# Optimization experiments

Hardware: AMD Instinct MI355X
Metric: run time of the kernel (lower is better)

Reference implementation:

```python
import jax, jax.numpy as jnp
import numpy as np

H = 16  # num_heads
D = 1024  # hidden_dim
HD = D // H  # head_dim


def setup_inputs() -> dict:
    key = jax.random.key(0)
    ks = jax.random.split(key, 12)
    B, S = 2, 2048
    x = jax.random.normal(ks[0], (B, S, D), dtype=jnp.float32)
    attention_bias = jax.random.normal(ks[1], (H, S, S), dtype=jnp.float32) * 0.1
    # padding mask: True = masked; last (S - len) positions padded, no all-masked rows
    lengths = jax.random.randint(ks[2], (B,), S // 2, S + 1)
    key_padding_mask = jnp.arange(S)[None, :] >= lengths[:, None]  # [B, S] bool
    s = 1.0 / np.sqrt(D)
    Wq = jax.random.normal(ks[3], (D, D), dtype=jnp.float32) * s
    bq = jnp.zeros((D,), dtype=jnp.float32)
    Wk = jax.random.normal(ks[4], (D, D), dtype=jnp.float32) * s
    bk = jnp.zeros((D,), dtype=jnp.float32)
    Wv = jax.random.normal(ks[5], (D, D), dtype=jnp.float32) * s
    bv = jnp.zeros((D,), dtype=jnp.float32)
    Wo = jax.random.normal(ks[6], (D, D), dtype=jnp.float32) * s
    bo = jnp.zeros((D,), dtype=jnp.float32)
    return {"x": x, "attention_bias": attention_bias, "key_padding_mask": key_padding_mask,
            "Wq": Wq, "bq": bq, "Wk": Wk, "bk": bk, "Wv": Wv, "bv": bv, "Wo": Wo, "bo": bo}


def reference(x, attention_bias, key_padding_mask, Wq, bq, Wk, bk, Wv, bv, Wo, bo):
    B, S, _ = x.shape
    scale = HD ** (-0.5)

    def shape_heads(t):  # [B,S,D] -> [B,H,S,HD]
        return t.reshape(B, S, H, HD).transpose(0, 2, 1, 3)

    q = shape_heads(x @ Wq + bq)
    k = shape_heads(x @ Wk + bk)
    v = shape_heads(x @ Wv + bv)

    attn = jnp.einsum('bhqd,bhkd->bhqk', q, k) * scale  # [B,H,S,S]
    attn = attn + attention_bias[None]
    attn = jnp.where(key_padding_mask[:, None, None, :], -jnp.inf, attn)

    # handle fully-masked rows: zero their logits pre-softmax, zero weights after
    all_masked = jnp.all(key_padding_mask, axis=1)  # [B]
    bad = all_masked[:, None, None, None]
    safe_attn = jnp.where(bad, 0.0, attn)
    weights = jax.nn.softmax(safe_attn, axis=-1)
    weights = jnp.where(bad, 0.0, weights)

    context = jnp.einsum('bhqk,bhkd->bhqd', weights, v)  # [B,H,S,HD]
    context = context.transpose(0, 2, 1, 3).reshape(B, S, D)
    return context @ Wo + bo
```

## Files before the change

kernel.cpp:

```cpp
#include <hip/hip_runtime.h>
#include <hip/hip_bf16.h>
#include <stdint.h>

#define BB 2
#define SS 2048
#define DDIM 1024
#define HH 16
#define HDIM 64

typedef __hip_bfloat16 bf16;
typedef __bf16 bf16x8 __attribute__((ext_vector_type(8)));
typedef float f32x4 __attribute__((ext_vector_type(4)));
typedef short short8 __attribute__((ext_vector_type(8)));
typedef short s16x4 __attribute__((ext_vector_type(4)));

static __device__ __forceinline__ f32x4 mfma16(bf16x8 a, bf16x8 b, f32x4 c) {
  return __builtin_amdgcn_mfma_f32_16x16x32_bf16(a, b, c, 0, 0, 0);
}

static __device__ __forceinline__ void gload_lds16(const void* g, void* l) {
  __builtin_amdgcn_global_load_lds(
      (const __attribute__((address_space(1))) void*)g,
      (__attribute__((address_space(3))) void*)l, 16, 0, 0);
}

__global__ __launch_bounds__(256) void cvt_k(const float* __restrict__ src,
                                             bf16* __restrict__ dst) {
  const int base = (blockIdx.x * 256 + threadIdx.x) * 8;
  float4 a = *reinterpret_cast<const float4*>(src + base);
  float4 b = *reinterpret_cast<const float4*>(src + base + 4);
  union {
    bf16 h[8];
    short8 v;
  } u;
  u.h[0] = __float2bfloat16(a.x);
  u.h[1] = __float2bfloat16(a.y);
  u.h[2] = __float2bfloat16(a.z);
  u.h[3] = __float2bfloat16(a.w);
  u.h[4] = __float2bfloat16(b.x);
  u.h[5] = __float2bfloat16(b.y);
  u.h[6] = __float2bfloat16(b.z);
  u.h[7] = __float2bfloat16(b.w);
  *reinterpret_cast<short8*>(dst + base) = u.v;
}

__global__ __launch_bounds__(256) void transpose_cvt_k(
    const float* __restrict__ src, bf16* __restrict__ dst) {
  __shared__ float tile[64][65];
  const int t = threadIdx.x;
  const int r = t >> 2, c0 = (t & 3) * 16;
  const int bx = blockIdx.x * 64, by = blockIdx.y * 64;
  const float* sp = src + (size_t)(by + r) * DDIM + bx + c0;
#pragma unroll
  for (int j = 0; j < 16; ++j) tile[r][c0 + j] = sp[j];
  __syncthreads();
  bf16* dp = dst + (size_t)(bx + r) * DDIM + by + c0;
#pragma unroll
  for (int j = 0; j < 16; ++j) dp[j] = __float2bfloat16(tile[c0 + j][r]);
}

__global__ __launch_bounds__(64) void mask_pack_k(
    const int* __restrict__ kpm, unsigned long long* __restrict__ mb) {
  const int i = threadIdx.x;
  const int b = i >> 5, c = i & 31;
  unsigned long long bits = 0ull;
  for (int j = 0; j < 64; ++j)
    bits |= (unsigned long long)(kpm[b * SS + c * 64 + j] != 0) << j;
  mb[i] = bits;
}

template <int MODE>
__global__ __launch_bounds__(256, 2) void gemm_bt(
    const bf16* __restrict__ A, const bf16* __restrict__ Bt,
    const float* __restrict__ b0, const float* __restrict__ b1,
    const float* __restrict__ b2, bf16* __restrict__ O0,
    bf16* __restrict__ O1, bf16* __restrict__ O2, float* __restrict__ Of) {
  constexpr int Kd = DDIM;
  __shared__ bf16x8 lA[128 * 8];
  __shared__ bf16x8 lB[128 * 8];
  const int tid = threadIdx.x;
  const int wave = tid >> 6, lane = tid & 63;
  const int l15 = lane & 15, l4 = lane >> 4;
  const int wm = wave >> 1, wn = wave & 1;
  const int m0 = blockIdx.x * 128, n0 = blockIdx.y * 128;
  const f32x4 z = {0.f, 0.f, 0.f, 0.f};
  f32x4 acc[4][4];
#pragma unroll
  for (int i = 0; i < 4; ++i)
#pragma unroll
    for (int j = 0; j < 4; ++j) acc[i][j] = z;

  for (int k0 = 0; k0 < Kd; k0 += 64) {
#pragma unroll
    for (int j = 0; j < 4; ++j) {
      const int slot = j * 256 + tid;
      const int r = slot >> 3, cs = slot & 7;
      const int c = cs ^ (r & 7);
      gload_lds16(A + (size_t)(m0 + r) * Kd + k0 + c * 8,
                  &lA[j * 256 + wave * 64]);
      gload_lds16(Bt + (size_t)(n0 + r) * Kd + k0 + c * 8,
                  &lB[j * 256 + wave * 64]);
    }
    __syncthreads();
    bf16x8 af[2][4], bfr[2][4];
#pragma unroll
    for (int ks = 0; ks < 2; ++ks) {
#pragma unroll
      for (int i = 0; i < 4; ++i) {
        const int ra = wm * 64 + i * 16 + l15;
        af[ks][i] = lA[ra * 8 + ((ks * 4 + l4) ^ (ra & 7))];
        const int rb = wn * 64 + i * 16 + l15;
        bfr[ks][i] = lB[rb * 8 + ((ks * 4 + l4) ^ (rb & 7))];
      }
    }
#pragma unroll
    for (int ks = 0; ks < 2; ++ks)
#pragma unroll
      for (int i = 0; i < 4; ++i)
#pragma unroll
        for (int j = 0; j < 4; ++j)
          acc[i][j] = mfma16(af[ks][i], bfr[ks][j], acc[i][j]);
    __syncthreads();
  }

#pragma unroll
  for (int i = 0; i < 4; ++i) {
    const int m = m0 + wm * 64 + i * 16 + l4 * 4;
#pragma unroll
    for (int j = 0; j < 4; ++j) {
      const int n = n0 + wn * 64 + j * 16 + l15;
      if (MODE == 1) {
        const float bb = b0[n];
#pragma unroll
        for (int r = 0; r < 4; ++r)
          Of[(size_t)(m + r) * DDIM + n] = acc[i][j][r] + bb;
      } else {
        const int sel = n >> 10, nn = n & 1023;
        const int h = nn >> 6, d = nn & 63;
        const float* bp = sel == 0 ? b0 : (sel == 1 ? b1 : b2);
        const float bb = bp[nn];
        const int b = m >> 11, s = m & 2047;
        if (sel == 2) {
          union {
            bf16 h4[4];
            s16x4 v;
          } u;
#pragma unroll
          for (int r = 0; r < 4; ++r)
            u.h4[r] = __float2bfloat16(acc[i][j][r] + bb);
          *reinterpret_cast<s16x4*>(
              &O2[((size_t)(b * HH + h) * HDIM + d) * SS + s]) = u.v;
        } else {
#pragma unroll
          for (int r = 0; r < 4; ++r) {
            const float val = acc[i][j][r] + bb;
            (sel ? O1 : O0)[((size_t)(b * HH + h) * SS + (s + r)) * HDIM + d] =
                __float2bfloat16(val);
          }
        }
      }
    }
  }
}

__global__ __launch_bounds__(256, 2) void attn_k(
    const bf16* __restrict__ Qb, const bf16* __restrict__ Kb,
    const bf16* __restrict__ Vt, const float* __restrict__ bias,
    const unsigned long long* __restrict__ mbits, bf16* __restrict__ ctx) {
  __shared__ bf16x8 lK[2][512];
  __shared__ bf16x8 lV[2][512];
  __shared__ unsigned int plP[4 * 512];
  const int tid = threadIdx.x;
  const int wave = tid >> 6, lane = tid & 63;
  const int l15 = lane & 15, l4 = lane >> 4;
  const int bid = ((blockIdx.x & 7) << 7) | (blockIdx.x >> 3);
  const int qblk = bid & 31, bh = bid >> 5;
  const int b = bh >> 4, h = bh & 15;
  const int q0b = qblk * 64;
  const int q0w = q0b + wave * 16;

  const bf16* Qp = Qb + ((size_t)bh * SS + q0w) * HDIM;
  const bf16* Kp = Kb + (size_t)bh * SS * HDIM;
  const bf16* Vp = Vt + (size_t)bh * HDIM * SS;
  const float* Bp = bias + (size_t)h * SS * SS + (size_t)(q0w + l15) * SS;
  unsigned int* plw = plP + wave * 512;

  const int rk0 = tid >> 3, ck0 = tid & 7;
  const int rk1 = 32 + rk0, ck1 = ck0;
  const int dk0 = rk0 * 8 + (ck0 ^ (rk0 & 7));
  const int dk1 = rk1 * 8 + (ck1 ^ (rk1 & 7));

  {
    bf16x8 k0 = *reinterpret_cast<const bf16x8*>(Kp + (size_t)rk0 * HDIM + ck0 * 8);
    bf16x8 k1 = *reinterpret_cast<const bf16x8*>(Kp + (size_t)rk1 * HDIM + ck1 * 8);
    bf16x8 v0 = *reinterpret_cast<const bf16x8*>(Vp + (size_t)rk0 * SS + ck0 * 8);
    bf16x8 v1 = *reinterpret_cast<const bf16x8*>(Vp + (size_t)rk1 * SS + ck1 * 8);
    lK[0][dk0] = k0;
    lK[0][dk1] = k1;
    lV[0][dk0] = v0;
    lV[0][dk1] = v1;
  }
  f32x4 bA0 = *reinterpret_cast<const f32x4*>(Bp + 0 * 16 + l4 * 4);
  f32x4 bA1 = *reinterpret_cast<const f32x4*>(Bp + 1 * 16 + l4 * 4);
  f32x4 bA2 = *reinterpret_cast<const f32x4*>(Bp + 2 * 16 + l4 * 4);
  f32x4 bA3 = *reinterpret_cast<const f32x4*>(Bp + 3 * 16 + l4 * 4);
  f32x4 bB0 = bA0, bB1 = bA1, bB2 = bA2, bB3 = bA3;

  bf16x8 qf[2];
#pragma unroll
  for (int ks = 0; ks < 2; ++ks)
    qf[ks] = *reinterpret_cast<const bf16x8*>(Qp + (size_t)l15 * HDIM +
                                              ks * 32 + l4 * 8);
  const f32x4 z = {0.f, 0.f, 0.f, 0.f};
  f32x4 o[4];
#pragma unroll
  for (int dd = 0; dd < 4; ++dd) o[dd] = z;
  float mrow = -1e30f, lrow = 0.f;

  __syncthreads();

#define JJROW(JJ, BC)                                                     \
  {                                                                       \
    const unsigned nib = (unsigned)(mb >> ((JJ)*16 + l4 * 4)) & 15u;      \
    _Pragma("unroll") for (int r = 0; r < 4; ++r) {                       \
      const float a = ((nib >> r) & 1u) ? -1e30f : (BC)[r];               \
      v[JJ][r] = fmaf(sc[JJ][r], 0.125f, a);                              \
      bm = fmaxf(bm, v[JJ][r]);                                           \
    }                                                                     \
  }

#define STEP(T, BC0, BC1, BC2, BC3, BN0, BN1, BN2, BN3)                        \
  {                                                                            \
    const int cur = (T)&1;                                                     \
    const int kbn = ((T) + 1) * 64;                                            \
    const bool pf = (T) < 31;                                                  \
    bf16x8 ks0, ks1, vs0, vs1;                                                 \
    if (pf) {                                                                  \
      ks0 = *reinterpret_cast<const bf16x8*>(Kp + (size_t)(kbn + rk0) * HDIM + \
                                             ck0 * 8);                         \
      ks1 = *reinterpret_cast<const bf16x8*>(Kp + (size_t)(kbn + rk1) * HDIM + \
                                             ck1 * 8);                         \
      vs0 = *reinterpret_cast<const bf16x8*>(Vp + (size_t)rk0 * SS + kbn +     \
                                             ck0 * 8);                         \
      vs1 = *reinterpret_cast<const bf16x8*>(Vp + (size_t)rk1 * SS + kbn +     \
                                             ck1 * 8);                         \
      BN0 = *reinterpret_cast<const f32x4*>(Bp + kbn + 0 * 16 + l4 * 4);       \
      BN1 = *reinterpret_cast<const f32x4*>(Bp + kbn + 1 * 16 + l4 * 4);       \
      BN2 = *reinterpret_cast<const f32x4*>(Bp + kbn + 2 * 16 + l4 * 4);       \
      BN3 = *reinterpret_cast<const f32x4*>(Bp + kbn + 3 * 16 + l4 * 4);       \
    }                                                                          \
    f32x4 sc[4];                                                               \
    _Pragma("unroll") for (int jj = 0; jj < 4; ++jj) {                         \
      const int R = jj * 16 + l15;                                             \
      bf16x8 kf0 = lK[cur][R * 8 + ((0 + l4) ^ (R & 7))];                      \
      bf16x8 kf1 = lK[cur][R * 8 + ((4 + l4) ^ (R & 7))];                      \
      f32x4 s = mfma16(kf0, qf[0], z);                                         \
      s = mfma16(kf1, qf[1], s);                                               \
      sc[jj] = s;                                                              \
    }                                                                          \
    const unsigned long long mb = mbits[(b << 5) + (T)];                       \
    float v[4][4];                                                             \
    float bm = -1e30f;                                                         \
    JJROW(0, BC0)                                                              \
    JJROW(1, BC1)                                                              \
    JJROW(2, BC2)                                                              \
    JJROW(3, BC3)                                                              \
    bm = fmaxf(bm, __shfl_xor(bm, 16));                                        \
    bm = fmaxf(bm, __shfl_xor(bm, 32));                                        \
    const float mn = fmaxf(mrow, bm);                                          \
    const float alpha = __expf(mrow - mn);                                     \
    mrow = mn;                                                                 \
    float ps = 0.f;                                                            \
    float p[4][4];                                                             \
    _Pragma("unroll") for (int jj = 0; jj < 4; ++jj)                           \
        _Pragma("unroll") for (int r = 0; r < 4; ++r) {                        \
      p[jj][r] = __expf(v[jj][r] - mn);                                        \
      ps += p[jj][r];                                                          \
    }                                                                          \
    ps += __shfl_xor(ps, 16);                                                  \
    ps += __shfl_xor(ps, 32);                                                  \
    lrow = lrow * alpha + ps;                                                  \
    _Pragma("unroll") for (int jj = 0; jj < 4; ++jj)                           \
        _Pragma("unroll") for (int r0 = 0; r0 < 4; r0 += 2) {                  \
      union {                                                                  \
        bf16 h2[2];                                                            \
        unsigned int w;                                                        \
      } u;                                                                     \
      u.h2[0] = __float2bfloat16(p[jj][r0]);                                   \
      u.h2[1] = __float2bfloat16(p[jj][r0 + 1]);                               \
      const int byte =                                                         \
          (l15 * 128 + jj * 32 + l4 * 8 + r0 * 2) ^ ((l15 & 7) << 4);          \
      plw[byte >> 2] = u.w;                                                    \
    }                                                                          \
    asm volatile("s_waitcnt lgkmcnt(0)" ::: "memory");                         \
    bf16x8 pfr[2];                                                             \
    _Pragma("unroll") for (int ks = 0; ks < 2; ++ks) {                         \
      const int byte = (l15 * 128 + ks * 64 + l4 * 16) ^ ((l15 & 7) << 4);     \
      pfr[ks] = *reinterpret_cast<const bf16x8*>(                              \
          reinterpret_cast<const char*>(plw) + byte);                          \
    }                                                                          \
    float ar[4];                                                               \
    _Pragma("unroll") for (int r = 0; r < 4; ++r) ar[r] =                      \
        __shfl(alpha, l4 * 4 + r);                                             \
    _Pragma("unroll") for (int dd = 0; dd < 4; ++dd) {                         \
      const int D = dd * 16 + l15;                                             \
      bf16x8 vf0 = lV[cur][D * 8 + ((0 + l4) ^ (D & 7))];                      \
      bf16x8 vf1 = lV[cur][D * 8 + ((4 + l4) ^ (D & 7))];                      \
      _Pragma("unroll") for (int r = 0; r < 4; ++r) o[dd][r] *= ar[r];         \
      o[dd] = mfma16(pfr[0], vf0, o[dd]);                                      \
      o[dd] = mfma16(pfr[1], vf1, o[dd]);                                      \
    }                                                                          \
    if (pf) {                                                                  \
      const int nxt = cur ^ 1;                                                 \
      lK[nxt][dk0] = ks0;                                                      \
      lK[nxt][dk1] = ks1;                                                      \
      lV[nxt][dk0] = vs0;                                                      \
      lV[nxt][dk1] = vs1;                                                      \
    }                                                                          \
    __syncthreads();                                                           \
  }

  for (int t2 = 0; t2 < 16; ++t2) {
    const int te = t2 * 2;
    STEP(te, bA0, bA1, bA2, bA3, bB0, bB1, bB2, bB3)
    STEP(te + 1, bB0, bB1, bB2, bB3, bA0, bA1, bA2, bA3)
  }
#undef STEP
#undef JJROW

  const float rl = 1.0f / lrow;
  float rlr[4];
#pragma unroll
  for (int r = 0; r < 4; ++r) rlr[r] = __shfl(rl, l4 * 4 + r);
#pragma unroll
  for (int dd = 0; dd < 4; ++dd) {
#pragma unroll
    for (int r = 0; r < 4; ++r) {
      const float val = o[dd][r] * rlr[r];
      const int s = q0w + l4 * 4 + r;
      ctx[((size_t)b * SS + s) * DDIM + h * HDIM + dd * 16 + l15] =
          __float2bfloat16(val);
    }
  }
}

extern "C" void kernel_launch(void* const* d_in, const int* in_sizes, int n_in,
                              void* d_out, int out_size, void* d_ws,
                              size_t ws_size, hipStream_t stream) {
  const float* x = (const float*)d_in[0];
  const float* abias = (const float*)d_in[1];
  const int* kpm = (const int*)d_in[2];
  const float* Wq = (const float*)d_in[3];
  const float* bq = (const float*)d_in[4];
  const float* Wk = (const float*)d_in[5];
  const float* bk = (const float*)d_in[6];
  const float* Wv = (const float*)d_in[7];
  const float* bv = (const float*)d_in[8];
  const float* Wo = (const float*)d_in[9];
  const float* bo = (const float*)d_in[10];
  float* out = (float*)d_out;

  char* ws = (char*)d_ws;
  bf16* xb = (bf16*)ws;
  bf16* Wt = (bf16*)(ws + 8388608);
  bf16* Wot = (bf16*)(ws + 14680064);
  bf16* Qb = (bf16*)(ws + 16777216);
  bf16* Kb = (bf16*)(ws + 25165824);
  bf16* Vtb = (bf16*)(ws + 33554432);
  bf16* ctx = (bf16*)(ws + 41943040);
  unsigned long long* mbits =
      (unsigned long long*)(ws + 50331648);

  dim3 t256(256);
  cvt_k<<<dim3(2048), t256, 0, stream>>>(x, xb);
  transpose_cvt_k<<<dim3(16, 16), t256, 0, stream>>>(Wq, Wt);
  transpose_cvt_k<<<dim3(16, 16), t256, 0, stream>>>(Wk, Wt + 1024 * 1024);
  transpose_cvt_k<<<dim3(16, 16), t256, 0, stream>>>(Wv, Wt + 2 * 1024 * 1024);
  transpose_cvt_k<<<dim3(16, 16), t256, 0, stream>>>(Wo, Wot);
  mask_pack_k<<<dim3(1), dim3(64), 0, stream>>>(kpm, mbits);

  gemm_bt<0><<<dim3(32, 24), t256, 0, stream>>>(xb, Wt, bq, bk, bv, Qb, Kb,
                                                Vtb, nullptr);
  attn_k<<<dim3(1024), t256, 0, stream>>>(Qb, Kb, Vtb, abias, mbits, ctx);
  gemm_bt<1><<<dim3(32, 8), t256, 0, stream>>>(ctx, Wot, bo, nullptr, nullptr,
                                               nullptr, nullptr, nullptr, out);
}
```

Baseline: 199.1 us.

## Use direct global-to-LDS loads in attention, lazy softmax rescale, merge prep kernels

The attention kernel now stages K/V tiles with direct global-to-LDS loads (pre-swizzled source addresses) instead of going through registers, and issues them after the current tile's fragments are read. Online softmax skips rescaling unless some row max grows by more than a threshold, which saves exp and multiply work but lets unnormalised values grow up to e^8 in fp32. The four weight transpose launches are merged into one 3D-grid launch, and mask packing uses a wave ballot across 64 blocks. Together these cut register pressure, VALU work and launch overhead, at the cost of relying on the global-to-LDS layout and the sync ordering being correct.

```diff
diff --git a/kernel.cpp b/kernel.cpp
--- a/kernel.cpp
+++ b/kernel.cpp
@@ -44,9 +44,15 @@
   *reinterpret_cast<short8*>(dst + base) = u.v;
 }
 
-__global__ __launch_bounds__(256) void transpose_cvt_k(
-    const float* __restrict__ src, bf16* __restrict__ dst) {
+__global__ __launch_bounds__(256) void transpose_cvt4_k(
+    const float* __restrict__ s0, const float* __restrict__ s1,
+    const float* __restrict__ s2, const float* __restrict__ s3,
+    bf16* __restrict__ d0, bf16* __restrict__ d1, bf16* __restrict__ d2,
+    bf16* __restrict__ d3) {
   __shared__ float tile[64][65];
+  const int zi = blockIdx.z;
+  const float* src = zi == 0 ? s0 : (zi == 1 ? s1 : (zi == 2 ? s2 : s3));
+  bf16* dst = zi == 0 ? d0 : (zi == 1 ? d1 : (zi == 2 ? d2 : d3));
   const int t = threadIdx.x;
   const int r = t >> 2, c0 = (t & 3) * 16;
   const int bx = blockIdx.x * 64, by = blockIdx.y * 64;
@@ -61,12 +67,11 @@
 
 __global__ __launch_bounds__(64) void mask_pack_k(
     const int* __restrict__ kpm, unsigned long long* __restrict__ mb) {
-  const int i = threadIdx.x;
+  const int i = blockIdx.x;
   const int b = i >> 5, c = i & 31;
-  unsigned long long bits = 0ull;
-  for (int j = 0; j < 64; ++j)
-    bits |= (unsigned long long)(kpm[b * SS + c * 64 + j] != 0) << j;
-  mb[i] = bits;
+  const unsigned long long bits =
+      __ballot(kpm[b * SS + c * 64 + threadIdx.x] != 0);
+  if (threadIdx.x == 0) mb[i] = bits;
 }
 
 template <int MODE>
@@ -185,21 +190,14 @@
   const float* Bp = bias + (size_t)h * SS * SS + (size_t)(q0w + l15) * SS;
   unsigned int* plw = plP + wave * 512;
 
-  const int rk0 = tid >> 3, ck0 = tid & 7;
-  const int rk1 = 32 + rk0, ck1 = ck0;
-  const int dk0 = rk0 * 8 + (ck0 ^ (rk0 & 7));
-  const int dk1 = rk1 * 8 + (ck1 ^ (rk1 & 7));
-
-  {
-    bf16x8 k0 = *reinterpret_cast<const bf16x8*>(Kp + (size_t)rk0 * HDIM + ck0 * 8);
-    bf16x8 k1 = *reinterpret_cast<const bf16x8*>(Kp + (size_t)rk1 * HDIM + ck1 * 8);
-    bf16x8 v0 = *reinterpret_cast<const bf16x8*>(Vp + (size_t)rk0 * SS + ck0 * 8);
-    bf16x8 v1 = *reinterpret_cast<const bf16x8*>(Vp + (size_t)rk1 * SS + ck1 * 8);
-    lK[0][dk0] = k0;
-    lK[0][dk1] = k1;
-    lV[0][dk0] = v0;
-    lV[0][dk1] = v1;
-  }
+  const int rs0 = tid >> 3, cs0 = (tid & 7) ^ (rs0 & 7);
+  const int rs1 = 32 + rs0, cs1 = (tid & 7) ^ (rs1 & 7);
+
+  gload_lds16(Kp + (size_t)rs0 * HDIM + cs0 * 8, &lK[0][wave * 64]);
+  gload_lds16(Kp + (size_t)rs1 * HDIM + cs1 * 8, &lK[0][256 + wave * 64]);
+  gload_lds16(Vp + (size_t)rs0 * SS + cs0 * 8, &lV[0][wave * 64]);
+  gload_lds16(Vp + (size_t)rs1 * SS + cs1 * 8, &lV[0][256 + wave * 64]);
+
   f32x4 bA0 = *reinterpret_cast<const f32x4*>(Bp + 0 * 16 + l4 * 4);
   f32x4 bA1 = *reinterpret_cast<const f32x4*>(Bp + 1 * 16 + l4 * 4);
   f32x4 bA2 = *reinterpret_cast<const f32x4*>(Bp + 2 * 16 + l4 * 4);
@@ -232,18 +230,10 @@
 #define STEP(T, BC0, BC1, BC2, BC3, BN0, BN1, BN2, BN3)                        \
   {                                                                            \
     const int cur = (T)&1;                                                     \
+    const int nxt = cur ^ 1;                                                   \
     const int kbn = ((T) + 1) * 64;                                            \
     const bool pf = (T) < 31;                                                  \
-    bf16x8 ks0, ks1, vs0, vs1;                                                 \
     if (pf) {                                                                  \
-      ks0 = *reinterpret_cast<const bf16x8*>(Kp + (size_t)(kbn + rk0) * HDIM + \
-                                             ck0 * 8);                         \
-      ks1 = *reinterpret_cast<const bf16x8*>(Kp + (size_t)(kbn + rk1) * HDIM + \
-                                             ck1 * 8);                         \
-      vs0 = *reinterpret_cast<const bf16x8*>(Vp + (size_t)rk0 * SS + kbn +     \
-                                             ck0 * 8);                         \
-      vs1 = *reinterpret_cast<const bf16x8*>(Vp + (size_t)rk1 * SS + kbn +     \
-                                             ck1 * 8);                         \
       BN0 = *reinterpret_cast<const f32x4*>(Bp + kbn + 0 * 16 + l4 * 4);       \
       BN1 = *reinterpret_cast<const f32x4*>(Bp + kbn + 1 * 16 + l4 * 4);       \
       BN2 = *reinterpret_cast<const f32x4*>(Bp + kbn + 2 * 16 + l4 * 4);       \
@@ -257,6 +247,12 @@
       f32x4 s = mfma16(kf0, qf[0], z);                                         \
       s = mfma16(kf1, qf[1], s);                                               \
       sc[jj] = s;                                                              \
+    }                                                                          \
+    if (pf) {                            \
+      gload_lds16(Kp + (size_t)(kbn + rs0) * HDIM + cs0 * 8,                   \
+                  &lK[nxt][wave * 64]);                                        \
+      gload_lds16(Kp + (size_t)(kbn + rs1) * HDIM + cs1 * 8,                   \
+                  &lK[nxt][256 + wave * 64]);                                  \
     }                                                                          \
     const unsigned long long mb = mbits[(b << 5) + (T)];                       \
     float v[4][4];                                                             \
@@ -267,14 +263,18 @@
     JJROW(3, BC3)                                                              \
     bm = fmaxf(bm, __shfl_xor(bm, 16));                                        \
     bm = fmaxf(bm, __shfl_xor(bm, 32));                                        \
-    const float mn = fmaxf(mrow, bm);                                          \
-    const float alpha = __expf(mrow - mn);                                     \
-    mrow = mn;                                                                 \
+    const bool resc = __any(bm > mrow + 8.0f);                                 \
+    float alpha = 1.0f;                                                        \
+    if (resc) {                                                                \
+      const float mn = fmaxf(mrow, bm);                                        \
+      alpha = __expf(mrow - mn);                                               \
+      mrow = mn;                                                               \
+    }                                                                          \
     float ps = 0.f;                                                            \
     float p[4][4];                                                             \
     _Pragma("unroll") for (int jj = 0; jj < 4; ++jj)                           \
         _Pragma("unroll") for (int r = 0; r < 4; ++r) {                        \
-      p[jj][r] = __expf(v[jj][r] - mn);                                        \
+      p[jj][r] = __expf(v[jj][r] - mrow);                                      \
       ps += p[jj][r];                                                          \
     }                                                                          \
     ps += __shfl_xor(ps, 16);                                                  \
@@ -292,6 +292,18 @@
           (l15 * 128 + jj * 32 + l4 * 8 + r0 * 2) ^ ((l15 & 7) << 4);          \
       plw[byte >> 2] = u.w;                                                    \
     }                                                                          \
+    bf16x8 vfr[4][2];                                                          \
+    _Pragma("unroll") for (int dd = 0; dd < 4; ++dd) {                         \
+      const int D = dd * 16 + l15;                                             \
+      vfr[dd][0] = lV[cur][D * 8 + ((0 + l4) ^ (D & 7))];                      \
+      vfr[dd][1] = lV[cur][D * 8 + ((4 + l4) ^ (D & 7))];                      \
+    }                                                                          \
+    if (pf) {                            \
+      gload_lds16(Vp + (size_t)rs0 * SS + kbn + cs0 * 8,                       \
+                  &lV[nxt][wave * 64]);                                        \
+      gload_lds16(Vp + (size_t)rs1 * SS + kbn + cs1 * 8,                       \
+                  &lV[nxt][256 + wave * 64]);                                  \
+    }                                                                          \
     asm volatile("s_waitcnt lgkmcnt(0)" ::: "memory");                         \
     bf16x8 pfr[2];                                                             \
     _Pragma("unroll") for (int ks = 0; ks < 2; ++ks) {                         \
@@ -299,23 +311,21 @@
       pfr[ks] = *reinterpret_cast<const bf16x8*>(                              \
           reinterpret_cast<const char*>(plw) + byte);                          \
     }                                                                          \
-    float ar[4];                                                               \
-    _Pragma("unroll") for (int r = 0; r < 4; ++r) ar[r] =                      \
-        __shfl(alpha, l4 * 4 + r);                                             \
+    if (resc) {                                                                \
+      float ar0 = __shfl(alpha, l4 * 4 + 0);                                   \
+      float ar1 = __shfl(alpha, l4 * 4 + 1);                                   \
+      float ar2 = __shfl(alpha, l4 * 4 + 2);                                   \
+      float ar3 = __shfl(alpha, l4 * 4 + 3);                                   \
+      _Pragma("unroll") for (int dd = 0; dd < 4; ++dd) {                       \
+        o[dd][0] *= ar0;                                                       \
+        o[dd][1] *= ar1;                                                       \
+        o[dd][2] *= ar2;                                                       \
+        o[dd][3] *= ar3;                                                       \
+      }                                                                        \
+    }                                                                          \
     _Pragma("unroll") for (int dd = 0; dd < 4; ++dd) {                         \
-      const int D = dd * 16 + l15;                                             \
-      bf16x8 vf0 = lV[cur][D * 8 + ((0 + l4) ^ (D & 7))];                      \
-      bf16x8 vf1 = lV[cur][D * 8 + ((4 + l4) ^ (D & 7))];                      \
-      _Pragma("unroll") for (int r = 0; r < 4; ++r) o[dd][r] *= ar[r];         \
-      o[dd] = mfma16(pfr[0], vf0, o[dd]);                                      \
-      o[dd] = mfma16(pfr[1], vf1, o[dd]);                                      \
-    }                                                                          \
-    if (pf) {                                                                  \
-      const int nxt = cur ^ 1;                                                 \
-      lK[nxt][dk0] = ks0;                                                      \
-      lK[nxt][dk1] = ks1;                                                      \
-      lV[nxt][dk0] = vs0;                                                      \
-      lV[nxt][dk1] = vs1;                                                      \
+      o[dd] = mfma16(pfr[0], vfr[dd][0], o[dd]);                               \
+      o[dd] = mfma16(pfr[1], vfr[dd][1], o[dd]);                               \
     }                                                                          \
     __syncthreads();                                                           \
   }
@@ -373,11 +383,9 @@
 
   dim3 t256(256);
   cvt_k<<<dim3(2048), t256, 0, stream>>>(x, xb);
-  transpose_cvt_k<<<dim3(16, 16), t256, 0, stream>>>(Wq, Wt);
-  transpose_cvt_k<<<dim3(16, 16), t256, 0, stream>>>(Wk, Wt + 1024 * 1024);
-  transpose_cvt_k<<<dim3(16, 16), t256, 0, stream>>>(Wv, Wt + 2 * 1024 * 1024);
-  transpose_cvt_k<<<dim3(16, 16), t256, 0, stream>>>(Wo, Wot);
-  mask_pack_k<<<dim3(1), dim3(64), 0, stream>>>(kpm, mbits);
+  transpose_cvt4_k<<<dim3(16, 16, 4), t256, 0, stream>>>(
+      Wq, Wk, Wv, Wo, Wt, Wt + 1024 * 1024, Wt + 2 * 1024 * 1024, Wot);
+  mask_pack_k<<<dim3(64), dim3(64), 0, stream>>>(kpm, mbits);
 
   gemm_bt<0><<<dim3(32, 24), t256, 0, stream>>>(xb, Wt, bq, bk, bv, Qb, Kb,
                                                 Vtb, nullptr);
```

New measurement: 191.1 us. 4.0% less time.
